# Performance work log

Hardware: AMD Instinct MI355X
Metric: run time of the kernel (lower is better)

## Reference

```python
import jax, jax.numpy as jnp
import numpy as np

B, V, M, C = 1024, 2, 256, 256  # batch, num_vars (must be 2), latent states, categories


def setup_inputs() -> dict:
    key = jax.random.key(0)
    k1, k2, k3 = jax.random.split(key, 3)
    x = jax.random.randint(k1, (B, V), 0, C)
    # input-node tables: per var v, per latent node k, a [M, C] row-normalized table
    W = jax.nn.softmax(jax.random.normal(k2, (V, M, M, C), dtype=jnp.float32), axis=-1)
    # sum-node mixture weights over the M product children
    w_sum = jax.nn.softmax(jax.random.normal(k3, (M,), dtype=jnp.float32))
    return {"x": x, "W": W, "w_sum": w_sum}


def reference(x, W, w_sum):
    # lp[v] has shape [M(k), M(m), B]: log W[v, k, m, x[b, v]]
    # (matches torch: probs[:, x_var].log() per input node, stacked over latent k)
    lp0 = jnp.log(W[0][:, :, x[:, 0]])  # [M, M, B]
    lp1 = jnp.log(W[1][:, :, x[:, 1]])  # [M, M, B]
    prod = lp0 + lp1                    # product nodes, [M(k), M, B]
    # sum node: log( sum_k w_k * exp(prod_k) ) -> [M, B]
    mixed = jnp.log(jnp.einsum('k,kmb->mb', w_sum, jnp.exp(prod)))
    # root: logsumexp over the leading M dim -> [B]
    return jax.nn.logsumexp(mixed, axis=0)
```

## Files before the change

### kernel.cpp

```cpp
#include <hip/hip_runtime.h>
#include <math.h>


#define KCHUNK 256
#define BK     32
#define NITER  (KCHUNK / BK)
#define LDSS   40

typedef float  f32x4  __attribute__((ext_vector_type(4)));
typedef short  bf16x8 __attribute__((ext_vector_type(8)));

static __device__ __forceinline__ short f2bf(float f) {
    unsigned u = __builtin_bit_cast(unsigned, f);
    u += 0x7fffu + ((u >> 16) & 1u);
    return (short)(u >> 16);
}

__global__ __launch_bounds__(512, 2) void gemm_gather_kernel(
    const int* __restrict__ x, const float* __restrict__ W,
    const float* __restrict__ wsum, float* __restrict__ G)
{
    extern __shared__ char smem[];
    short* __restrict__ As = (short*)smem;
    short* __restrict__ Bs = (short*)(smem + 256 * LDSS * 2);
    float* __restrict__ Sg = (float*)smem;

    const int  split = blockIdx.x;
    const long kbase = (long)split * KCHUNK;
    const float* __restrict__ Ag = W + kbase * 256;
    const float* __restrict__ Bg = W + 16777216 + kbase * 256;

    const int t  = threadIdx.x;
    const int cq = (t & 63) * 4;
    const int kq = (t >> 6) * 4;

    const int lane = t & 63;
    const int wv   = t >> 6;
    const int wc0  = (wv & 3) * 64;
    const int wc1  = (wv >> 2) * 128;
    const int ml   = lane & 15;
    const int qd   = lane >> 4;

    f32x4 acc[4][8];
#pragma unroll
    for (int i = 0; i < 4; ++i)
#pragma unroll
        for (int j = 0; j < 8; ++j) acc[i][j] = (f32x4){0.f, 0.f, 0.f, 0.f};

    for (int it = 0; it < NITER; ++it) {
        float4 a4[4], b4[4];
#pragma unroll
        for (int r = 0; r < 4; ++r) {
            a4[r] = *(const float4*)(Ag + (long)(it * BK + kq + r) * 256 + cq);
            b4[r] = *(const float4*)(Bg + (long)(it * BK + kq + r) * 256 + cq);
        }
        __syncthreads();
        const float* af = reinterpret_cast<const float*>(a4);
        const float* bf = reinterpret_cast<const float*>(b4);
#pragma unroll
        for (int j = 0; j < 4; ++j) {
            short4 av, bv;
            av.x = f2bf(af[0 * 4 + j]);
            av.y = f2bf(af[1 * 4 + j]);
            av.z = f2bf(af[2 * 4 + j]);
            av.w = f2bf(af[3 * 4 + j]);
            *(short4*)&As[(cq + j) * LDSS + kq] = av;
            bv.x = f2bf(bf[0 * 4 + j]);
            bv.y = f2bf(bf[1 * 4 + j]);
            bv.z = f2bf(bf[2 * 4 + j]);
            bv.w = f2bf(bf[3 * 4 + j]);
            *(short4*)&Bs[(cq + j) * LDSS + kq] = bv;
        }
        __syncthreads();
        bf16x8 afr[4];
#pragma unroll
        for (int mi = 0; mi < 4; ++mi)
            afr[mi] = *(const bf16x8*)&As[(wc0 + mi * 16 + ml) * LDSS + qd * 8];
#pragma unroll
        for (int ni = 0; ni < 8; ++ni) {
            const bf16x8 bfr = *(const bf16x8*)&Bs[(wc1 + ni * 16 + ml) * LDSS + qd * 8];
#pragma unroll
            for (int mi = 0; mi < 4; ++mi)
                acc[mi][ni] = __builtin_amdgcn_mfma_f32_16x16x32_bf16(
                    afr[mi], bfr, acc[mi][ni], 0, 0, 0);
        }
    }

    const int b0 = t, b1 = t + 512;
    const int2 xa = ((const int2*)x)[b0];
    const int2 xb = ((const int2*)x)[b1];
    float v0 = 0.f, v1 = 0.f;
#pragma unroll
    for (int q = 0; q < 4; ++q) {
        __syncthreads();
        if (wc0 == q * 64) {
#pragma unroll
            for (int mi = 0; mi < 4; ++mi)
#pragma unroll
                for (int ni = 0; ni < 8; ++ni)
#pragma unroll
                    for (int r = 0; r < 4; ++r)
                        Sg[(mi * 16 + qd * 4 + r) * 256 + wc1 + ni * 16 + ml] =
                            acc[mi][ni][r];
        }
        __syncthreads();
        if ((xa.x >> 6) == q) v0 = Sg[(xa.x & 63) * 256 + xa.y];
        if ((xb.x >> 6) == q) v1 = Sg[(xb.x & 63) * 256 + xb.y];
    }
    const float w = wsum[split];
    G[(long)b0 * 256 + split] = v0 * w;
    G[(long)b1 * 256 + split] = v1 * w;
}

__global__ __launch_bounds__(256) void finish_kernel(
    const float* __restrict__ G, float* __restrict__ out)
{
    const int b    = blockIdx.x * 4 + (threadIdx.x >> 6);
    const int lane = threadIdx.x & 63;
    const float4 g = ((const float4*)(G + (long)b * 256))[lane];
    float v = (g.x + g.y) + (g.z + g.w);
#pragma unroll
    for (int off = 32; off > 0; off >>= 1) v += __shfl_down(v, off);
    if (lane == 0) out[b] = logf(v);
}

extern "C" void kernel_launch(void* const* d_in, const int* in_sizes, int n_in,
                              void* d_out, int out_size, void* d_ws, size_t ws_size,
                              hipStream_t stream)
{
    const int*   x    = (const int*)d_in[0];
    const float* W    = (const float*)d_in[1];
    const float* wsum = (const float*)d_in[2];
    float* G   = (float*)d_ws;
    float* out = (float*)d_out;

    gemm_gather_kernel<<<dim3(256), 512, 65536, stream>>>(x, W, wsum, G);
    finish_kernel<<<dim3(256), 256, 0, stream>>>(G, out);
}
```

Baseline: 201.2 us.

## Load MFMA fragments directly from global memory, dropping LDS staging

The main loop no longer stages the bf16-converted A and B tiles through shared memory with two barriers per iteration. Each lane now loads the fp32 values it needs for its MFMA fragments straight from global memory with scalar strided loads, converts them in registers, and issues the MFMAs. B is handled in two halves to limit register pressure. This removes LDS traffic and barriers, but each element is now loaded by several waves (A by the two wc1 groups, B by the four wc0 groups). The loads are also 4-byte scalar, not float4, so global and L2 traffic and load instruction count rise.

```diff
diff --git a/kernel.cpp b/kernel.cpp
--- a/kernel.cpp
+++ b/kernel.cpp
@@ -5,7 +5,6 @@
 #define KCHUNK 256
 #define BK     32
 #define NITER  (KCHUNK / BK)
-#define LDSS   40
 
 typedef float  f32x4  __attribute__((ext_vector_type(4)));
 typedef short  bf16x8 __attribute__((ext_vector_type(8)));
@@ -16,13 +15,18 @@
     return (short)(u >> 16);
 }
 
+static __device__ __forceinline__ bf16x8 pack8(const float* f) {
+    bf16x8 r;
+#pragma unroll
+    for (int j = 0; j < 8; ++j) r[j] = f2bf(f[j]);
+    return r;
+}
+
 __global__ __launch_bounds__(512, 2) void gemm_gather_kernel(
     const int* __restrict__ x, const float* __restrict__ W,
     const float* __restrict__ wsum, float* __restrict__ G)
 {
     extern __shared__ char smem[];
-    short* __restrict__ As = (short*)smem;
-    short* __restrict__ Bs = (short*)(smem + 256 * LDSS * 2);
     float* __restrict__ Sg = (float*)smem;
 
     const int  split = blockIdx.x;
@@ -30,16 +34,17 @@
     const float* __restrict__ Ag = W + kbase * 256;
     const float* __restrict__ Bg = W + 16777216 + kbase * 256;
 
-    const int t  = threadIdx.x;
-    const int cq = (t & 63) * 4;
-    const int kq = (t >> 6) * 4;
-
+    const int t    = threadIdx.x;
     const int lane = t & 63;
     const int wv   = t >> 6;
     const int wc0  = (wv & 3) * 64;
     const int wc1  = (wv >> 2) * 128;
     const int ml   = lane & 15;
     const int qd   = lane >> 4;
+
+    const int b0 = t, b1 = t + 512;
+    const int2 xa = ((const int2*)x)[b0];
+    const int2 xb = ((const int2*)x)[b1];
 
     f32x4 acc[4][8];
 #pragma unroll
@@ -48,47 +53,52 @@
         for (int j = 0; j < 8; ++j) acc[i][j] = (f32x4){0.f, 0.f, 0.f, 0.f};
 
     for (int it = 0; it < NITER; ++it) {
-        float4 a4[4], b4[4];
+        const float* __restrict__ pA = Ag + ((long)it * BK + qd * 8) * 256;
+        const float* __restrict__ pB = Bg + ((long)it * BK + qd * 8) * 256;
+
+        float a[4][8];
 #pragma unroll
-        for (int r = 0; r < 4; ++r) {
-            a4[r] = *(const float4*)(Ag + (long)(it * BK + kq + r) * 256 + cq);
-            b4[r] = *(const float4*)(Bg + (long)(it * BK + kq + r) * 256 + cq);
-        }
-        __syncthreads();
-        const float* af = reinterpret_cast<const float*>(a4);
-        const float* bf = reinterpret_cast<const float*>(b4);
+        for (int mi = 0; mi < 4; ++mi)
 #pragma unroll
-        for (int j = 0; j < 4; ++j) {
-            short4 av, bv;
-            av.x = f2bf(af[0 * 4 + j]);
-            av.y = f2bf(af[1 * 4 + j]);
-            av.z = f2bf(af[2 * 4 + j]);
-            av.w = f2bf(af[3 * 4 + j]);
-            *(short4*)&As[(cq + j) * LDSS + kq] = av;
-            bv.x = f2bf(bf[0 * 4 + j]);
-            bv.y = f2bf(bf[1 * 4 + j]);
-            bv.z = f2bf(bf[2 * 4 + j]);
-            bv.w = f2bf(bf[3 * 4 + j]);
-            *(short4*)&Bs[(cq + j) * LDSS + kq] = bv;
-        }
-        __syncthreads();
+            for (int j = 0; j < 8; ++j)
+                a[mi][j] = pA[(long)j * 256 + wc0 + mi * 16 + ml];
+
+        float b[4][8];
+#pragma unroll
+        for (int ni = 0; ni < 4; ++ni)
+#pragma unroll
+            for (int j = 0; j < 8; ++j)
+                b[ni][j] = pB[(long)j * 256 + wc1 + ni * 16 + ml];
+
         bf16x8 afr[4];
 #pragma unroll
-        for (int mi = 0; mi < 4; ++mi)
-            afr[mi] = *(const bf16x8*)&As[(wc0 + mi * 16 + ml) * LDSS + qd * 8];
+        for (int mi = 0; mi < 4; ++mi) afr[mi] = pack8(a[mi]);
+
 #pragma unroll
-        for (int ni = 0; ni < 8; ++ni) {
-            const bf16x8 bfr = *(const bf16x8*)&Bs[(wc1 + ni * 16 + ml) * LDSS + qd * 8];
+        for (int ni = 0; ni < 4; ++ni) {
+            const bf16x8 bfr = pack8(b[ni]);
 #pragma unroll
             for (int mi = 0; mi < 4; ++mi)
                 acc[mi][ni] = __builtin_amdgcn_mfma_f32_16x16x32_bf16(
                     afr[mi], bfr, acc[mi][ni], 0, 0, 0);
         }
+
+#pragma unroll
+        for (int ni = 0; ni < 4; ++ni)
+#pragma unroll
+            for (int j = 0; j < 8; ++j)
+                b[ni][j] = pB[(long)j * 256 + wc1 + (ni + 4) * 16 + ml];
+
+#pragma unroll
+        for (int ni = 0; ni < 4; ++ni) {
+            const bf16x8 bfr = pack8(b[ni]);
+#pragma unroll
+            for (int mi = 0; mi < 4; ++mi)
+                acc[mi][ni + 4] = __builtin_amdgcn_mfma_f32_16x16x32_bf16(
+                    afr[mi], bfr, acc[mi][ni + 4], 0, 0, 0);
+        }
     }
 
-    const int b0 = t, b1 = t + 512;
-    const int2 xa = ((const int2*)x)[b0];
-    const int2 xb = ((const int2*)x)[b1];
     float v0 = 0.f, v1 = 0.f;
 #pragma unroll
     for (int q = 0; q < 4; ++q) {
```

New measurement: 320.8 us. 1.59x slower.

## Split GEMM output columns across two blocks per k-chunk to double the grid

Applied to the files above, without the earlier changes.

Each k-chunk block is split into two blocks along the second category dimension, giving a 2x256 grid. Each block computes half the output columns with half the accumulators and half the shared memory, and the gather and write are restricted to batch rows whose category falls in that half. Launch bounds are raised to allow more resident blocks per CU, aiming at better latency hiding and fuller CU use. In exchange, the A operand is read twice from global memory, and the tighter register budget may cause spills.

```diff
diff --git a/kernel.cpp b/kernel.cpp
--- a/kernel.cpp
+++ b/kernel.cpp
@@ -16,7 +16,7 @@
     return (short)(u >> 16);
 }
 
-__global__ __launch_bounds__(512, 2) void gemm_gather_kernel(
+__global__ __launch_bounds__(512, 4) void gemm_gather_kernel(
     const int* __restrict__ x, const float* __restrict__ W,
     const float* __restrict__ wsum, float* __restrict__ G)
 {
@@ -25,51 +25,59 @@
     short* __restrict__ Bs = (short*)(smem + 256 * LDSS * 2);
     float* __restrict__ Sg = (float*)smem;
 
-    const int  split = blockIdx.x;
+    const int  c1t   = blockIdx.x;
+    const int  split = blockIdx.y;
     const long kbase = (long)split * KCHUNK;
     const float* __restrict__ Ag = W + kbase * 256;
-    const float* __restrict__ Bg = W + 16777216 + kbase * 256;
+    const float* __restrict__ Bg = W + 16777216 + kbase * 256 + c1t * 128;
 
-    const int t  = threadIdx.x;
-    const int cq = (t & 63) * 4;
-    const int kq = (t >> 6) * 4;
+    const int t = threadIdx.x;
+    const int cqA = (t & 63) * 4;
+    const int kqA = (t >> 6) * 4;
+    const int cqB = (t & 31) * 4;
+    const int kqB = (t >> 5) * 2;
 
     const int lane = t & 63;
     const int wv   = t >> 6;
     const int wc0  = (wv & 3) * 64;
-    const int wc1  = (wv >> 2) * 128;
+    const int wc1  = (wv >> 2) * 64;
     const int ml   = lane & 15;
     const int qd   = lane >> 4;
 
-    f32x4 acc[4][8];
+    const int b0 = t, b1 = t + 512;
+    const int2 xa = ((const int2*)x)[b0];
+    const int2 xb = ((const int2*)x)[b1];
+
+    f32x4 acc[4][4];
 #pragma unroll
     for (int i = 0; i < 4; ++i)
 #pragma unroll
-        for (int j = 0; j < 8; ++j) acc[i][j] = (f32x4){0.f, 0.f, 0.f, 0.f};
+        for (int j = 0; j < 4; ++j) acc[i][j] = (f32x4){0.f, 0.f, 0.f, 0.f};
 
     for (int it = 0; it < NITER; ++it) {
-        float4 a4[4], b4[4];
+        const long k0 = (long)it * BK;
+        float4 a4[4], b4[2];
 #pragma unroll
-        for (int r = 0; r < 4; ++r) {
-            a4[r] = *(const float4*)(Ag + (long)(it * BK + kq + r) * 256 + cq);
-            b4[r] = *(const float4*)(Bg + (long)(it * BK + kq + r) * 256 + cq);
-        }
+        for (int r = 0; r < 4; ++r)
+            a4[r] = *(const float4*)(Ag + (k0 + kqA + r) * 256 + cqA);
+#pragma unroll
+        for (int r = 0; r < 2; ++r)
+            b4[r] = *(const float4*)(Bg + (k0 + kqB + r) * 256 + cqB);
         __syncthreads();
         const float* af = reinterpret_cast<const float*>(a4);
         const float* bf = reinterpret_cast<const float*>(b4);
 #pragma unroll
         for (int j = 0; j < 4; ++j) {
-            short4 av, bv;
+            short4 av;
             av.x = f2bf(af[0 * 4 + j]);
             av.y = f2bf(af[1 * 4 + j]);
             av.z = f2bf(af[2 * 4 + j]);
             av.w = f2bf(af[3 * 4 + j]);
-            *(short4*)&As[(cq + j) * LDSS + kq] = av;
+            *(short4*)&As[(cqA + j) * LDSS + kqA] = av;
+            short2 bv;
             bv.x = f2bf(bf[0 * 4 + j]);
             bv.y = f2bf(bf[1 * 4 + j]);
-            bv.z = f2bf(bf[2 * 4 + j]);
-            bv.w = f2bf(bf[3 * 4 + j]);
-            *(short4*)&Bs[(cq + j) * LDSS + kq] = bv;
+            *(short2*)&Bs[(cqB + j) * LDSS + kqB] = bv;
         }
         __syncthreads();
         bf16x8 afr[4];
@@ -77,7 +85,7 @@
         for (int mi = 0; mi < 4; ++mi)
             afr[mi] = *(const bf16x8*)&As[(wc0 + mi * 16 + ml) * LDSS + qd * 8];
 #pragma unroll
-        for (int ni = 0; ni < 8; ++ni) {
+        for (int ni = 0; ni < 4; ++ni) {
             const bf16x8 bfr = *(const bf16x8*)&Bs[(wc1 + ni * 16 + ml) * LDSS + qd * 8];
 #pragma unroll
             for (int mi = 0; mi < 4; ++mi)
@@ -86,30 +94,29 @@
         }
     }
 
-    const int b0 = t, b1 = t + 512;
-    const int2 xa = ((const int2*)x)[b0];
-    const int2 xb = ((const int2*)x)[b1];
+    const bool own0 = (xa.y >> 7) == c1t;
+    const bool own1 = (xb.y >> 7) == c1t;
     float v0 = 0.f, v1 = 0.f;
 #pragma unroll
     for (int q = 0; q < 4; ++q) {
         __syncthreads();
-        if (wc0 == q * 64) {
+        if ((wv & 3) == q) {
 #pragma unroll
             for (int mi = 0; mi < 4; ++mi)
 #pragma unroll
-                for (int ni = 0; ni < 8; ++ni)
+                for (int ni = 0; ni < 4; ++ni)
 #pragma unroll
                     for (int r = 0; r < 4; ++r)
-                        Sg[(mi * 16 + qd * 4 + r) * 256 + wc1 + ni * 16 + ml] =
+                        Sg[(mi * 16 + qd * 4 + r) * 128 + wc1 + ni * 16 + ml] =
                             acc[mi][ni][r];
         }
         __syncthreads();
-        if ((xa.x >> 6) == q) v0 = Sg[(xa.x & 63) * 256 + xa.y];
-        if ((xb.x >> 6) == q) v1 = Sg[(xb.x & 63) * 256 + xb.y];
+        if (own0 && (xa.x >> 6) == q) v0 = Sg[(xa.x & 63) * 128 + (xa.y & 127)];
+        if (own1 && (xb.x >> 6) == q) v1 = Sg[(xb.x & 63) * 128 + (xb.y & 127)];
     }
     const float w = wsum[split];
-    G[(long)b0 * 256 + split] = v0 * w;
-    G[(long)b1 * 256 + split] = v1 * w;
+    if (own0) G[(long)b0 * 256 + split] = v0 * w;
+    if (own1) G[(long)b1 * 256 + split] = v1 * w;
 }
 
 __global__ __launch_bounds__(256) void finish_kernel(
@@ -134,6 +141,6 @@
     float* G   = (float*)d_ws;
     float* out = (float*)d_out;
 
-    gemm_gather_kernel<<<dim3(256), 512, 65536, stream>>>(x, W, wsum, G);
+    gemm_gather_kernel<<<dim3(2, 256), 512, 32768, stream>>>(x, W, wsum, G);
     finish_kernel<<<dim3(256), 256, 0, stream>>>(G, out);
 }
```

After: 200.7 us. No clear change (-0.2%).
